# Performance work log

Measured on AMD Instinct MI355X. Metric: run time of the kernel, lower is better.

The kernel has to match this reference:

```python
import jax, jax.numpy as jnp
import numpy as np

B, S = 256, 512          # batch, seqlen
M = 128                  # memory_size
DK = 128                 # memory_key_state_dim == q_embed_dim == final_fc_dim
DV = 256                 # memory_value_state_dim == qa_embed_dim
NQ = 10000               # n_question
FC = 128                 # final_fc_dim


def _kaiming(key, shape):
    fan_in = shape[-1]
    return jax.random.normal(key, shape, dtype=jnp.float32) * np.float32(np.sqrt(2.0 / fan_in))


def setup_inputs() -> dict:
    key = jax.random.key(0)
    ks = jax.random.split(key, 12)
    q_data = jax.random.randint(ks[0], (B, S), 0, NQ + 1)
    qa_data = jax.random.randint(ks[1], (B, S), 0, 2 * NQ + 1)
    # embedding tables (padding_idx=0 -> zero row)
    q_embed_table = _kaiming(ks[2], (NQ + 1, DK)).at[0].set(0.0)
    qa_embed_table = _kaiming(ks[3], (2 * NQ + 1, DV)).at[0].set(0.0)
    memory_key = _kaiming(ks[4], (M, DK))
    init_memory_value = _kaiming(ks[5], (M, DV))
    W_erase = _kaiming(ks[6], (DV, DV)); b_erase = jnp.zeros((DV,), jnp.float32)
    W_add = _kaiming(ks[7], (DV, DV)); b_add = jnp.zeros((DV,), jnp.float32)
    W_read = _kaiming(ks[8], (FC, DV + FC)); b_read = jnp.zeros((FC,), jnp.float32)
    W_pred = _kaiming(ks[9], (1, FC)); b_pred = jnp.zeros((1,), jnp.float32)
    return {
        "q_data": q_data, "qa_data": qa_data,
        "q_embed_table": q_embed_table, "qa_embed_table": qa_embed_table,
        "memory_key": memory_key, "init_memory_value": init_memory_value,
        "W_erase": W_erase, "b_erase": b_erase,
        "W_add": W_add, "b_add": b_add,
        "W_read": W_read, "b_read": b_read,
        "W_pred": W_pred, "b_pred": b_pred,
    }


def reference(q_data, qa_data, q_embed_table, qa_embed_table, memory_key,
              init_memory_value, W_erase, b_erase, W_add, b_add,
              W_read, b_read, W_pred, b_pred):
    batch = q_data.shape[0]
    qe = q_embed_table[q_data]      # [B,S,DK]
    qae = qa_embed_table[qa_data]   # [B,S,DV]

    def step(mem, inp):
        q_t, qa_t = inp  # [B,DK], [B,DV]
        # key addressing: tiny matmul + softmax
        w = jax.nn.softmax(q_t @ memory_key.T, axis=1)            # [B,M]
        # weighted read from value memory
        read = jnp.einsum('bm,bmd->bd', w, mem)                   # [B,DV]
        # gated erase/add write
        e = jax.nn.sigmoid(qa_t @ W_erase.T + b_erase)            # [B,DV]
        a = jnp.tanh(qa_t @ W_add.T + b_add)                      # [B,DV]
        mem = mem * (1.0 - w[:, :, None] * e[:, None, :]) + w[:, :, None] * a[:, None, :]
        return mem, read

    mem0 = jnp.broadcast_to(init_memory_value, (batch,) + init_memory_value.shape)
    _, reads = jax.lax.scan(step, mem0, (qe.transpose(1, 0, 2), qae.transpose(1, 0, 2)))
    reads = reads.transpose(1, 0, 2)                              # [B,S,DV]

    predict_input = jnp.concatenate([reads, qe], axis=-1)         # [B,S,DV+FC]
    h = jnp.tanh(predict_input @ W_read.T + b_read)               # [B,S,FC]
    logits = h @ W_pred.T + b_pred                                # [B,S,1]
    return logits[..., 0]
```

## Files before the change

### kernel.cpp

```cpp
#include <hip/hip_runtime.h>
#include <hip/hip_bf16.h>


#define BB    256
#define SS    512
#define MM    128
#define DKk   128
#define DVv   256

typedef float  f32x2  __attribute__((ext_vector_type(2)));
typedef float  f32x4  __attribute__((ext_vector_type(4)));
typedef short  bf16x8 __attribute__((ext_vector_type(8)));

static __device__ __forceinline__ unsigned short f2bf(float f) {
    unsigned u = __float_as_uint(f);
    unsigned r = (u + 0x7FFFu + ((u >> 16) & 1u)) >> 16;
    return (unsigned short)r;
}
static __device__ __forceinline__ float fast_tanh(float x) {
    float ex = __expf(2.f * x);
    return 1.f - 2.f / (ex + 1.f);
}
static __device__ __forceinline__ float fast_sigmoid(float x) {
    return 1.f / (1.f + __expf(-x));
}

__global__ __launch_bounds__(256) void kt_transpose(const float* __restrict__ mk,
                                                    float* __restrict__ mkt) {
    int idx = blockIdx.x * 256 + threadIdx.x;
    int m = idx >> 7, k = idx & 127;
    mkt[(size_t)k * MM + m] = mk[(size_t)m * DKk + k];
}

__global__ __launch_bounds__(256) void kcvt(const float* __restrict__ qa_tab,
                                            const float* __restrict__ q_tab,
                                            const float* __restrict__ W_er,
                                            const float* __restrict__ W_ad,
                                            const float* __restrict__ W_rd,
                                            unsigned short* __restrict__ qa16,
                                            unsigned short* __restrict__ q16,
                                            unsigned short* __restrict__ wea16,
                                            unsigned short* __restrict__ wrd16,
                                            int n_qa, int n_q) {
    for (int i = blockIdx.x * 256 + threadIdx.x; i < n_qa; i += gridDim.x * 256)
        qa16[i] = f2bf(qa_tab[i]);
    for (int i = blockIdx.x * 256 + threadIdx.x; i < n_q; i += gridDim.x * 256)
        q16[i] = f2bf(q_tab[i]);
    for (int i = blockIdx.x * 256 + threadIdx.x; i < 65536; i += gridDim.x * 256) {
        wea16[i] = f2bf(W_er[i]);
        wea16[65536 + i] = f2bf(W_ad[i]);
    }
    for (int i = blockIdx.x * 256 + threadIdx.x; i < 49152; i += gridDim.x * 256)
        wrd16[i] = f2bf(W_rd[i]);
}

__global__ __launch_bounds__(256) void k1_scores(const int* __restrict__ q_data,
                                                 const float* __restrict__ q_tab,
                                                 const float* __restrict__ mkt,
                                                 float* __restrict__ w_buf,
                                                 int tcs, int tcm, int coff) {
    __shared__ float A[64][132];
    __shared__ int qidx[64];
    int t = threadIdx.x;
    int row0 = blockIdx.x * 64;
    if (t < 64) {
        int rl = row0 + t;
        qidx[t] = q_data[(rl >> tcs) * SS + coff + (rl & tcm)];
    }
    __syncthreads();
    #pragma unroll
    for (int i = 0; i < 8; ++i) {
        int f = t + 256 * i;
        int r = f >> 5, c4 = f & 31;
        float4 v = *reinterpret_cast<const float4*>(q_tab + (size_t)qidx[r] * DKk + c4 * 4);
        *reinterpret_cast<float4*>(&A[r][c4 * 4]) = v;
    }
    __syncthreads();
    int rg = t >> 4, cg = t & 15;
    float acc[4][8];
    #pragma unroll
    for (int i = 0; i < 4; ++i)
        #pragma unroll
        for (int j = 0; j < 8; ++j) acc[i][j] = 0.f;

    for (int k = 0; k < 128; k += 4) {
        float a_[4][4];
        #pragma unroll
        for (int i = 0; i < 4; ++i) {
            float4 v = *reinterpret_cast<const float4*>(&A[rg * 4 + i][k]);
            a_[i][0] = v.x; a_[i][1] = v.y; a_[i][2] = v.z; a_[i][3] = v.w;
        }
        #pragma unroll
        for (int kk = 0; kk < 4; ++kk) {
            const float* bp = mkt + (size_t)(k + kk) * MM + cg * 8;
            float4 b0 = *reinterpret_cast<const float4*>(bp);
            float4 b1 = *reinterpret_cast<const float4*>(bp + 4);
            #pragma unroll
            for (int i = 0; i < 4; ++i) {
                float av = a_[i][kk];
                acc[i][0] = fmaf(av, b0.x, acc[i][0]);
                acc[i][1] = fmaf(av, b0.y, acc[i][1]);
                acc[i][2] = fmaf(av, b0.z, acc[i][2]);
                acc[i][3] = fmaf(av, b0.w, acc[i][3]);
                acc[i][4] = fmaf(av, b1.x, acc[i][4]);
                acc[i][5] = fmaf(av, b1.y, acc[i][5]);
                acc[i][6] = fmaf(av, b1.z, acc[i][6]);
                acc[i][7] = fmaf(av, b1.w, acc[i][7]);
            }
        }
    }
    #pragma unroll
    for (int i = 0; i < 4; ++i) {
        float mx = acc[i][0];
        #pragma unroll
        for (int j = 1; j < 8; ++j) mx = fmaxf(mx, acc[i][j]);
        for (int off = 1; off < 16; off <<= 1) mx = fmaxf(mx, __shfl_xor(mx, off, 64));
        float s = 0.f;
        #pragma unroll
        for (int j = 0; j < 8; ++j) { float p = __expf(acc[i][j] - mx); acc[i][j] = p; s += p; }
        for (int off = 1; off < 16; off <<= 1) s += __shfl_xor(s, off, 64);
        float inv = 1.f / s;
        #pragma unroll
        for (int j = 0; j < 8; ++j) acc[i][j] *= inv;
        size_t ro = (size_t)(row0 + rg * 4 + i) * MM + cg * 8;
        *reinterpret_cast<float4*>(w_buf + ro)     = make_float4(acc[i][0], acc[i][1], acc[i][2], acc[i][3]);
        *reinterpret_cast<float4*>(w_buf + ro + 4) = make_float4(acc[i][4], acc[i][5], acc[i][6], acc[i][7]);
    }
}

__global__ __launch_bounds__(256) void k2_ea_mfma(const int* __restrict__ qa_data,
                                                  const unsigned short* __restrict__ qa16,
                                                  const unsigned short* __restrict__ wea16,
                                                  const float* __restrict__ b_er,
                                                  const float* __restrict__ b_ad,
                                                  float* __restrict__ ea_buf,
                                                  int tcs, int tcm, int coff) {
    __shared__ __align__(16) unsigned short A_lds[128 * 64];
    __shared__ int qidx[128];
    int t = threadIdx.x;
    int rb = blockIdx.x >> 2, cb = blockIdx.x & 3;
    int row0 = rb * 128;
    if (t < 128) {
        int rl = row0 + t;
        qidx[t] = qa_data[(rl >> tcs) * SS + coff + (rl & tcm)];
    }
    int l = t & 63;
    int wid = t >> 6, wr = wid >> 1, wc = wid & 1;
    f32x4 acc[4][4];
    #pragma unroll
    for (int i = 0; i < 4; ++i)
        #pragma unroll
        for (int j = 0; j < 4; ++j)
            acc[i][j] = (f32x4){0.f, 0.f, 0.f, 0.f};

    for (int ks = 0; ks < 256; ks += 64) {
        __syncthreads();
        #pragma unroll
        for (int p = 0; p < 4; ++p) {
            int U = p * 256 + t;
            int r = U >> 3, kb = U & 7;
            int kb_log = kb ^ (r & 7);
            int4 v = *reinterpret_cast<const int4*>(qa16 + (size_t)qidx[r] * 256 + ks + kb_log * 8);
            *reinterpret_cast<int4*>(&A_lds[U * 8]) = v;
        }
        __syncthreads();
        #pragma unroll
        for (int ksub = 0; ksub < 2; ++ksub) {
            bf16x8 af[4];
            #pragma unroll
            for (int mi = 0; mi < 4; ++mi) {
                int r = wr * 64 + mi * 16 + (l & 15);
                int kb_log = ksub * 4 + (l >> 4);
                int pu = r * 8 + (kb_log ^ (r & 7));
                af[mi] = *reinterpret_cast<const bf16x8*>(&A_lds[pu * 8]);
            }
            #pragma unroll
            for (int nj = 0; nj < 4; ++nj) {
                int col = cb * 128 + wc * 64 + nj * 16 + (l & 15);
                bf16x8 bf = *reinterpret_cast<const bf16x8*>(
                    wea16 + (size_t)col * 256 + ks + ksub * 32 + (l >> 4) * 8);
                #pragma unroll
                for (int mi = 0; mi < 4; ++mi)
                    acc[mi][nj] = __builtin_amdgcn_mfma_f32_16x16x32_bf16(af[mi], bf, acc[mi][nj], 0, 0, 0);
            }
        }
    }
    #pragma unroll
    for (int nj = 0; nj < 4; ++nj) {
        int col = cb * 128 + wc * 64 + nj * 16 + (l & 15);
        bool is_e = (cb < 2);
        float bias = is_e ? b_er[col] : b_ad[col - 256];
        #pragma unroll
        for (int mi = 0; mi < 4; ++mi) {
            #pragma unroll
            for (int reg = 0; reg < 4; ++reg) {
                int rl = row0 + wr * 64 + mi * 16 + (l >> 4) * 4 + reg;
                float x = acc[mi][nj][reg] + bias;
                float y = is_e ? fast_sigmoid(x) : fast_tanh(x);
                ea_buf[(size_t)rl * 512 + col] = y;
            }
        }
    }
}

__global__ __launch_bounds__(1024, 1) void k3_seq(const float* __restrict__ w_buf,
                                                  const float* __restrict__ ea_buf,
                                                  const float* __restrict__ init_mem,
                                                  float* __restrict__ state,
                                                  unsigned short* __restrict__ reads16,
                                                  int TC, int first, int last) {
    __shared__ float wlds[2][8][128];
    __shared__ float rdlds[8][4][256];
    int b = blockIdx.x;
    int tid = threadIdx.x;
    int wv = tid >> 6, lane = tid & 63;
    int mq = wv >> 2, dq = wv & 3;
    int d = dq * 64 + lane;
    int m0 = mq * 32;
    f32x2 mem[16];
    if (first) {
        #pragma unroll
        for (int i = 0; i < 16; ++i) {
            mem[i].x = init_mem[(size_t)(m0 + 2 * i) * DVv + d];
            mem[i].y = init_mem[(size_t)(m0 + 2 * i + 1) * DVv + d];
        }
    } else {
        #pragma unroll
        for (int i = 0; i < 16; ++i)
            mem[i] = *reinterpret_cast<const f32x2*>(&state[((size_t)b * DVv + d) * MM + m0 + 2 * i]);
    }
    size_t rb = (size_t)b * TC;
    int gg = tid >> 7, mm = tid & 127;
    wlds[0][gg][mm] = w_buf[(rb + gg) * MM + mm];
    __syncthreads();
    for (int t0 = 0; t0 < TC; t0 += 8) {
        int cur = (t0 >> 3) & 1, nxt = cur ^ 1;
        bool havenext = (t0 + 8) < TC;
        float wn = 0.f;
        if (havenext) wn = w_buf[(rb + t0 + 8 + gg) * MM + mm];
        float e8[8], a8[8];
        #pragma unroll
        for (int g = 0; g < 8; ++g) {
            size_t rr = (rb + t0 + g) * 512;
            e8[g] = ea_buf[rr + d];
            a8[g] = ea_buf[rr + 256 + d];
        }
        #pragma unroll
        for (int g = 0; g < 8; ++g) {
            const f32x4* wp4 = reinterpret_cast<const f32x4*>(&wlds[cur][g][m0]);
            f32x2 rd; rd.x = 0.f; rd.y = 0.f;
            f32x2 ne2; ne2.x = -e8[g]; ne2.y = -e8[g];
            f32x2 a2;  a2.x = a8[g];  a2.y = a8[g];
            #pragma unroll
            for (int j = 0; j < 8; ++j) {
                f32x4 w4 = wp4[j];
                f32x2 wlo; wlo.x = w4.x; wlo.y = w4.y;
                f32x2 whi; whi.x = w4.z; whi.y = w4.w;
                f32x2 tt;
                asm("v_pk_fma_f32 %0, %1, %2, %0" : "+v"(rd)          : "v"(wlo), "v"(mem[2*j]));
                asm("v_pk_fma_f32 %0, %1, %2, %3" : "=v"(tt)          : "v"(ne2), "v"(mem[2*j]), "v"(a2));
                asm("v_pk_fma_f32 %0, %1, %2, %0" : "+v"(mem[2*j])    : "v"(wlo), "v"(tt));
                asm("v_pk_fma_f32 %0, %1, %2, %0" : "+v"(rd)          : "v"(whi), "v"(mem[2*j+1]));
                asm("v_pk_fma_f32 %0, %1, %2, %3" : "=v"(tt)          : "v"(ne2), "v"(mem[2*j+1]), "v"(a2));
                asm("v_pk_fma_f32 %0, %1, %2, %0" : "+v"(mem[2*j+1])  : "v"(whi), "v"(tt));
            }
            rdlds[g][mq][d] = rd.x + rd.y;
        }
        __syncthreads();
        if (havenext) wlds[nxt][gg][mm] = wn;
        #pragma unroll
        for (int r = 0; r < 2; ++r) {
            int idx = tid + r * 1024;
            int g = idx >> 8, dd = idx & 255;
            float s = rdlds[g][0][dd] + rdlds[g][1][dd] + rdlds[g][2][dd] + rdlds[g][3][dd];
            reads16[(rb + t0 + g) * DVv + dd] = f2bf(s);
        }
        __syncthreads();
    }
    if (!last) {
        #pragma unroll
        for (int i = 0; i < 16; ++i)
            *reinterpret_cast<f32x2*>(&state[((size_t)b * DVv + d) * MM + m0 + 2 * i]) = mem[i];
    }
}

__global__ __launch_bounds__(256) void k4_mfma(const int* __restrict__ q_data,
                                               const unsigned short* __restrict__ q16,
                                               const unsigned short* __restrict__ reads16,
                                               const unsigned short* __restrict__ wrd16,
                                               const float* __restrict__ b_rd,
                                               const float* __restrict__ W_pr,
                                               const float* __restrict__ b_pr,
                                               float* __restrict__ out,
                                               int tcs, int tcm, int coff) {
    __shared__ __align__(16) unsigned short A_lds[128 * 64];
    __shared__ int qidx[128];
    __shared__ float plds[2][128];
    int t = threadIdx.x;
    int row0 = blockIdx.x * 128;
    if (t < 128) {
        int rl = row0 + t;
        qidx[t] = q_data[(rl >> tcs) * SS + coff + (rl & tcm)];
    }
    int l = t & 63;
    int wid = t >> 6, wr = wid >> 1, wc = wid & 1;
    f32x4 acc[4][4];
    #pragma unroll
    for (int i = 0; i < 4; ++i)
        #pragma unroll
        for (int j = 0; j < 4; ++j)
            acc[i][j] = (f32x4){0.f, 0.f, 0.f, 0.f};

    for (int ks = 0; ks < 384; ks += 64) {
        __syncthreads();
        #pragma unroll
        for (int p = 0; p < 4; ++p) {
            int U = p * 256 + t;
            int r = U >> 3, kb = U & 7;
            int kb_log = kb ^ (r & 7);
            int kg = ks + kb_log * 8;
            const unsigned short* src = (kg < 256)
                ? (reads16 + (size_t)(row0 + r) * DVv + kg)
                : (q16 + (size_t)qidx[r] * DKk + (kg - 256));
            int4 v = *reinterpret_cast<const int4*>(src);
            *reinterpret_cast<int4*>(&A_lds[U * 8]) = v;
        }
        __syncthreads();
        #pragma unroll
        for (int ksub = 0; ksub < 2; ++ksub) {
            bf16x8 af[4];
            #pragma unroll
            for (int mi = 0; mi < 4; ++mi) {
                int r = wr * 64 + mi * 16 + (l & 15);
                int kb_log = ksub * 4 + (l >> 4);
                int pu = r * 8 + (kb_log ^ (r & 7));
                af[mi] = *reinterpret_cast<const bf16x8*>(&A_lds[pu * 8]);
            }
            #pragma unroll
            for (int nj = 0; nj < 4; ++nj) {
                int col = wc * 64 + nj * 16 + (l & 15);
                bf16x8 bf = *reinterpret_cast<const bf16x8*>(
                    wrd16 + (size_t)col * 384 + ks + ksub * 32 + (l >> 4) * 8);
                #pragma unroll
                for (int mi = 0; mi < 4; ++mi)
                    acc[mi][nj] = __builtin_amdgcn_mfma_f32_16x16x32_bf16(af[mi], bf, acc[mi][nj], 0, 0, 0);
            }
        }
    }
    float part[16];
    #pragma unroll
    for (int k = 0; k < 16; ++k) part[k] = 0.f;
    #pragma unroll
    for (int nj = 0; nj < 4; ++nj) {
        int col = wc * 64 + nj * 16 + (l & 15);
        float bias = b_rd[col];
        float wpr = W_pr[col];
        #pragma unroll
        for (int mi = 0; mi < 4; ++mi) {
            #pragma unroll
            for (int reg = 0; reg < 4; ++reg) {
                float h = fast_tanh(acc[mi][nj][reg] + bias);
                part[mi * 4 + reg] = fmaf(h, wpr, part[mi * 4 + reg]);
            }
        }
    }
    #pragma unroll
    for (int k = 0; k < 16; ++k) {
        #pragma unroll
        for (int off = 1; off < 16; off <<= 1)
            part[k] += __shfl_xor(part[k], off, 64);
    }
    if ((l & 15) == 0) {
        #pragma unroll
        for (int mi = 0; mi < 4; ++mi)
            #pragma unroll
            for (int reg = 0; reg < 4; ++reg) {
                int row = wr * 64 + mi * 16 + (l >> 4) * 4 + reg;
                plds[wc][row] = part[mi * 4 + reg];
            }
    }
    __syncthreads();
    if (t < 128) {
        float s = plds[0][t] + plds[1][t] + b_pr[0];
        int rl = row0 + t;
        out[(rl >> tcs) * SS + coff + (rl & tcm)] = s;
    }
}

extern "C" void kernel_launch(void* const* d_in, const int* in_sizes, int n_in,
                              void* d_out, int out_size, void* d_ws, size_t ws_size,
                              hipStream_t stream) {
    const int*   q_data   = (const int*)d_in[0];
    const int*   qa_data  = (const int*)d_in[1];
    const float* q_tab    = (const float*)d_in[2];
    const float* qa_tab   = (const float*)d_in[3];
    const float* mk       = (const float*)d_in[4];
    const float* init_mem = (const float*)d_in[5];
    const float* W_er     = (const float*)d_in[6];
    const float* b_er     = (const float*)d_in[7];
    const float* W_ad     = (const float*)d_in[8];
    const float* b_ad     = (const float*)d_in[9];
    const float* W_rd     = (const float*)d_in[10];
    const float* b_rd     = (const float*)d_in[11];
    const float* W_pr     = (const float*)d_in[12];
    const float* b_pr     = (const float*)d_in[13];
    float* out = (float*)d_out;

    const size_t state_f = (size_t)BB * MM * DVv;
    const size_t qa16_n  = (size_t)in_sizes[3];
    const size_t q16_n   = (size_t)in_sizes[2];
    const size_t wea16_n = 131072;
    const size_t wrd16_n = 49152;
    const size_t bf16_f  = (qa16_n + q16_n + wea16_n + wrd16_n) / 2 + 16;

    size_t avail_f = ws_size / 4;
    int TC = 8;
    {
        const int cand[] = {512, 256, 128, 64, 32, 16, 8};
        for (int i = 0; i < 7; ++i) {
            size_t need = 16384 + state_f + bf16_f + (size_t)BB * cand[i] * (MM + 512 + 128);
            if (need <= avail_f) { TC = cand[i]; break; }
        }
    }
    int NC = SS / TC;
    int tcs = __builtin_ctz(TC);
    int tcm = TC - 1;

    float* ws      = (float*)d_ws;
    float* mkt     = ws;
    float* state   = mkt + 16384;
    float* w_buf   = state + state_f;
    float* ea_buf  = w_buf + (size_t)BB * TC * MM;
    unsigned short* reads16 = (unsigned short*)(ea_buf + (size_t)BB * TC * 512);
    unsigned short* qa16  = reads16 + (size_t)BB * TC * DVv;
    unsigned short* q16   = qa16 + qa16_n;
    unsigned short* wea16 = q16 + q16_n;
    unsigned short* wrd16 = wea16 + wea16_n;

    kt_transpose<<<64, 256, 0, stream>>>(mk, mkt);
    kcvt<<<1024, 256, 0, stream>>>(qa_tab, q_tab, W_er, W_ad, W_rd, qa16, q16, wea16, wrd16,
                                   (int)qa16_n, (int)q16_n);
    for (int c = 0; c < NC; ++c) {
        int coff = c * TC;
        int rows = BB * TC;
        k1_scores<<<rows / 64, 256, 0, stream>>>(q_data, q_tab, mkt, w_buf, tcs, tcm, coff);
        k2_ea_mfma<<<(rows / 128) * 4, 256, 0, stream>>>(qa_data, qa16, wea16, b_er, b_ad,
                                                         ea_buf, tcs, tcm, coff);
        k3_seq<<<BB, 1024, 0, stream>>>(w_buf, ea_buf, init_mem, state, reads16,
                                        TC, c == 0, c == NC - 1);
        k4_mfma<<<rows / 128, 256, 0, stream>>>(q_data, q16, reads16, wrd16, b_rd, W_pr, b_pr,
                                                out, tcs, tcm, coff);
    }
}
```

Measured before the change: 625.9 us.

## Use MFMA for key scores, bf16 erase/add buffer, readlane weights in scan

```diff
diff --git a/kernel.cpp b/kernel.cpp
--- a/kernel.cpp
+++ b/kernel.cpp
@@ -17,19 +17,15 @@
     unsigned r = (u + 0x7FFFu + ((u >> 16) & 1u)) >> 16;
     return (unsigned short)r;
 }
+static __device__ __forceinline__ float bf2f(unsigned short u) {
+    return __uint_as_float(((unsigned)u) << 16);
+}
 static __device__ __forceinline__ float fast_tanh(float x) {
     float ex = __expf(2.f * x);
     return 1.f - 2.f / (ex + 1.f);
 }
 static __device__ __forceinline__ float fast_sigmoid(float x) {
     return 1.f / (1.f + __expf(-x));
-}
-
-__global__ __launch_bounds__(256) void kt_transpose(const float* __restrict__ mk,
-                                                    float* __restrict__ mkt) {
-    int idx = blockIdx.x * 256 + threadIdx.x;
-    int m = idx >> 7, k = idx & 127;
-    mkt[(size_t)k * MM + m] = mk[(size_t)m * DKk + k];
 }
 
 __global__ __launch_bounds__(256) void kcvt(const float* __restrict__ qa_tab,
@@ -37,10 +33,12 @@
                                             const float* __restrict__ W_er,
                                             const float* __restrict__ W_ad,
                                             const float* __restrict__ W_rd,
+                                            const float* __restrict__ mk,
                                             unsigned short* __restrict__ qa16,
                                             unsigned short* __restrict__ q16,
                                             unsigned short* __restrict__ wea16,
                                             unsigned short* __restrict__ wrd16,
+                                            unsigned short* __restrict__ mk16,
                                             int n_qa, int n_q) {
     for (int i = blockIdx.x * 256 + threadIdx.x; i < n_qa; i += gridDim.x * 256)
         qa16[i] = f2bf(qa_tab[i]);
@@ -52,79 +50,84 @@
     }
     for (int i = blockIdx.x * 256 + threadIdx.x; i < 49152; i += gridDim.x * 256)
         wrd16[i] = f2bf(W_rd[i]);
-}
-
-__global__ __launch_bounds__(256) void k1_scores(const int* __restrict__ q_data,
-                                                 const float* __restrict__ q_tab,
-                                                 const float* __restrict__ mkt,
-                                                 float* __restrict__ w_buf,
-                                                 int tcs, int tcm, int coff) {
-    __shared__ float A[64][132];
-    __shared__ int qidx[64];
+    for (int i = blockIdx.x * 256 + threadIdx.x; i < 16384; i += gridDim.x * 256)
+        mk16[i] = f2bf(mk[i]);
+}
+
+__global__ __launch_bounds__(256) void k1_mfma(const int* __restrict__ q_data,
+                                               const unsigned short* __restrict__ q16,
+                                               const unsigned short* __restrict__ mk16,
+                                               float* __restrict__ w_buf,
+                                               int tcs, int tcm, int coff) {
+    __shared__ __align__(16) unsigned short A_lds[128 * 64];
+    __shared__ int qidx[128];
     int t = threadIdx.x;
-    int row0 = blockIdx.x * 64;
-    if (t < 64) {
+    int row0 = blockIdx.x * 128;
+    if (t < 128) {
         int rl = row0 + t;
         qidx[t] = q_data[(rl >> tcs) * SS + coff + (rl & tcm)];
     }
-    __syncthreads();
-    #pragma unroll
-    for (int i = 0; i < 8; ++i) {
-        int f = t + 256 * i;
-        int r = f >> 5, c4 = f & 31;
-        float4 v = *reinterpret_cast<const float4*>(q_tab + (size_t)qidx[r] * DKk + c4 * 4);
-        *reinterpret_cast<float4*>(&A[r][c4 * 4]) = v;
-    }
-    __syncthreads();
-    int rg = t >> 4, cg = t & 15;
-    float acc[4][8];
-    #pragma unroll
-    for (int i = 0; i < 4; ++i)
-        #pragma unroll
-        for (int j = 0; j < 8; ++j) acc[i][j] = 0.f;
-
-    for (int k = 0; k < 128; k += 4) {
-        float a_[4][4];
-        #pragma unroll
-        for (int i = 0; i < 4; ++i) {
-            float4 v = *reinterpret_cast<const float4*>(&A[rg * 4 + i][k]);
-            a_[i][0] = v.x; a_[i][1] = v.y; a_[i][2] = v.z; a_[i][3] = v.w;
-        }
-        #pragma unroll
-        for (int kk = 0; kk < 4; ++kk) {
-            const float* bp = mkt + (size_t)(k + kk) * MM + cg * 8;
-            float4 b0 = *reinterpret_cast<const float4*>(bp);
-            float4 b1 = *reinterpret_cast<const float4*>(bp + 4);
-            #pragma unroll
-            for (int i = 0; i < 4; ++i) {
-                float av = a_[i][kk];
-                acc[i][0] = fmaf(av, b0.x, acc[i][0]);
-                acc[i][1] = fmaf(av, b0.y, acc[i][1]);
-                acc[i][2] = fmaf(av, b0.z, acc[i][2]);
-                acc[i][3] = fmaf(av, b0.w, acc[i][3]);
-                acc[i][4] = fmaf(av, b1.x, acc[i][4]);
-                acc[i][5] = fmaf(av, b1.y, acc[i][5]);
-                acc[i][6] = fmaf(av, b1.z, acc[i][6]);
-                acc[i][7] = fmaf(av, b1.w, acc[i][7]);
-            }
-        }
-    }
-    #pragma unroll
-    for (int i = 0; i < 4; ++i) {
-        float mx = acc[i][0];
-        #pragma unroll
-        for (int j = 1; j < 8; ++j) mx = fmaxf(mx, acc[i][j]);
-        for (int off = 1; off < 16; off <<= 1) mx = fmaxf(mx, __shfl_xor(mx, off, 64));
-        float s = 0.f;
-        #pragma unroll
-        for (int j = 0; j < 8; ++j) { float p = __expf(acc[i][j] - mx); acc[i][j] = p; s += p; }
-        for (int off = 1; off < 16; off <<= 1) s += __shfl_xor(s, off, 64);
-        float inv = 1.f / s;
-        #pragma unroll
-        for (int j = 0; j < 8; ++j) acc[i][j] *= inv;
-        size_t ro = (size_t)(row0 + rg * 4 + i) * MM + cg * 8;
-        *reinterpret_cast<float4*>(w_buf + ro)     = make_float4(acc[i][0], acc[i][1], acc[i][2], acc[i][3]);
-        *reinterpret_cast<float4*>(w_buf + ro + 4) = make_float4(acc[i][4], acc[i][5], acc[i][6], acc[i][7]);
+    int l = t & 63;
+    int wid = t >> 6;
+    f32x4 acc[2][8];
+    #pragma unroll
+    for (int i = 0; i < 2; ++i)
+        #pragma unroll
+        for (int j = 0; j < 8; ++j)
+            acc[i][j] = (f32x4){0.f, 0.f, 0.f, 0.f};
+
+    for (int ks = 0; ks < 128; ks += 64) {
+        __syncthreads();
+        #pragma unroll
+        for (int p = 0; p < 4; ++p) {
+            int U = p * 256 + t;
+            int r = U >> 3, kb = U & 7;
+            int kb_log = kb ^ (r & 7);
+            int4 v = *reinterpret_cast<const int4*>(q16 + (size_t)qidx[r] * DKk + ks + kb_log * 8);
+            *reinterpret_cast<int4*>(&A_lds[U * 8]) = v;
+        }
+        __syncthreads();
+        #pragma unroll
+        for (int ksub = 0; ksub < 2; ++ksub) {
+            bf16x8 af[2];
+            #pragma unroll
+            for (int mi = 0; mi < 2; ++mi) {
+                int r = wid * 32 + mi * 16 + (l & 15);
+                int kb_log = ksub * 4 + (l >> 4);
+                int pu = r * 8 + (kb_log ^ (r & 7));
+                af[mi] = *reinterpret_cast<const bf16x8*>(&A_lds[pu * 8]);
+            }
+            #pragma unroll
+            for (int nj = 0; nj < 8; ++nj) {
+                int col = nj * 16 + (l & 15);
+                bf16x8 bf = *reinterpret_cast<const bf16x8*>(
+                    mk16 + (size_t)col * DKk + ks + ksub * 32 + (l >> 4) * 8);
+                #pragma unroll
+                for (int mi = 0; mi < 2; ++mi)
+                    acc[mi][nj] = __builtin_amdgcn_mfma_f32_16x16x32_bf16(af[mi], bf, acc[mi][nj], 0, 0, 0);
+            }
+        }
+    }
+    #pragma unroll
+    for (int mi = 0; mi < 2; ++mi) {
+        #pragma unroll
+        for (int reg = 0; reg < 4; ++reg) {
+            float mx = acc[mi][0][reg];
+            #pragma unroll
+            for (int nj = 1; nj < 8; ++nj) mx = fmaxf(mx, acc[mi][nj][reg]);
+            #pragma unroll
+            for (int off = 1; off < 16; off <<= 1) mx = fmaxf(mx, __shfl_xor(mx, off, 64));
+            float p[8], s = 0.f;
+            #pragma unroll
+            for (int nj = 0; nj < 8; ++nj) { p[nj] = __expf(acc[mi][nj][reg] - mx); s += p[nj]; }
+            #pragma unroll
+            for (int off = 1; off < 16; off <<= 1) s += __shfl_xor(s, off, 64);
+            float inv = 1.f / s;
+            int row = row0 + wid * 32 + mi * 16 + (l >> 4) * 4 + reg;
+            #pragma unroll
+            for (int nj = 0; nj < 8; ++nj)
+                w_buf[(size_t)row * MM + nj * 16 + (l & 15)] = p[nj] * inv;
+        }
     }
 }
 
@@ -133,7 +136,7 @@
                                                   const unsigned short* __restrict__ wea16,
                                                   const float* __restrict__ b_er,
                                                   const float* __restrict__ b_ad,
-                                                  float* __restrict__ ea_buf,
+                                                  unsigned short* __restrict__ ea16,
                                                   int tcs, int tcm, int coff) {
     __shared__ __align__(16) unsigned short A_lds[128 * 64];
     __shared__ int qidx[128];
@@ -197,19 +200,18 @@
                 int rl = row0 + wr * 64 + mi * 16 + (l >> 4) * 4 + reg;
                 float x = acc[mi][nj][reg] + bias;
                 float y = is_e ? fast_sigmoid(x) : fast_tanh(x);
-                ea_buf[(size_t)rl * 512 + col] = y;
+                ea16[(size_t)rl * 512 + col] = f2bf(y);
             }
         }
     }
 }
 
 __global__ __launch_bounds__(1024, 1) void k3_seq(const float* __restrict__ w_buf,
-                                                  const float* __restrict__ ea_buf,
+                                                  const unsigned short* __restrict__ ea16,
                                                   const float* __restrict__ init_mem,
                                                   float* __restrict__ state,
                                                   unsigned short* __restrict__ reads16,
                                                   int TC, int first, int last) {
-    __shared__ float wlds[2][8][128];
     __shared__ float rdlds[8][4][256];
     int b = blockIdx.x;
     int tid = threadIdx.x;
@@ -230,44 +232,36 @@
             mem[i] = *reinterpret_cast<const f32x2*>(&state[((size_t)b * DVv + d) * MM + m0 + 2 * i]);
     }
     size_t rb = (size_t)b * TC;
-    int gg = tid >> 7, mm = tid & 127;
-    wlds[0][gg][mm] = w_buf[(rb + gg) * MM + mm];
-    __syncthreads();
     for (int t0 = 0; t0 < TC; t0 += 8) {
-        int cur = (t0 >> 3) & 1, nxt = cur ^ 1;
-        bool havenext = (t0 + 8) < TC;
-        float wn = 0.f;
-        if (havenext) wn = w_buf[(rb + t0 + 8 + gg) * MM + mm];
+        f32x4 w4 = *reinterpret_cast<const f32x4*>(
+            w_buf + (rb + t0 + (lane >> 3)) * MM + m0 + (lane & 7) * 4);
         float e8[8], a8[8];
         #pragma unroll
         for (int g = 0; g < 8; ++g) {
-            size_t rr = (rb + t0 + g) * 512;
-            e8[g] = ea_buf[rr + d];
-            a8[g] = ea_buf[rr + 256 + d];
+            const unsigned short* ep = ea16 + (rb + t0 + g) * 512;
+            e8[g] = bf2f(ep[d]);
+            a8[g] = bf2f(ep[256 + d]);
         }
         #pragma unroll
         for (int g = 0; g < 8; ++g) {
-            const f32x4* wp4 = reinterpret_cast<const f32x4*>(&wlds[cur][g][m0]);
             f32x2 rd; rd.x = 0.f; rd.y = 0.f;
             f32x2 ne2; ne2.x = -e8[g]; ne2.y = -e8[g];
             f32x2 a2;  a2.x = a8[g];  a2.y = a8[g];
             #pragma unroll
-            for (int j = 0; j < 8; ++j) {
-                f32x4 w4 = wp4[j];
-                f32x2 wlo; wlo.x = w4.x; wlo.y = w4.y;
-                f32x2 whi; whi.x = w4.z; whi.y = w4.w;
+            for (int i = 0; i < 16; ++i) {
+                int src = 8 * g + (i >> 1);
+                int c = (i & 1) * 2;
+                f32x2 ws;
+                ws.x = __uint_as_float((unsigned)__builtin_amdgcn_readlane(__float_as_uint(w4[c]), src));
+                ws.y = __uint_as_float((unsigned)__builtin_amdgcn_readlane(__float_as_uint(w4[c + 1]), src));
                 f32x2 tt;
-                asm("v_pk_fma_f32 %0, %1, %2, %0" : "+v"(rd)          : "v"(wlo), "v"(mem[2*j]));
-                asm("v_pk_fma_f32 %0, %1, %2, %3" : "=v"(tt)          : "v"(ne2), "v"(mem[2*j]), "v"(a2));
-                asm("v_pk_fma_f32 %0, %1, %2, %0" : "+v"(mem[2*j])    : "v"(wlo), "v"(tt));
-                asm("v_pk_fma_f32 %0, %1, %2, %0" : "+v"(rd)          : "v"(whi), "v"(mem[2*j+1]));
-                asm("v_pk_fma_f32 %0, %1, %2, %3" : "=v"(tt)          : "v"(ne2), "v"(mem[2*j+1]), "v"(a2));
-                asm("v_pk_fma_f32 %0, %1, %2, %0" : "+v"(mem[2*j+1])  : "v"(whi), "v"(tt));
+                asm("v_pk_fma_f32 %0, %1, %2, %0" : "+v"(rd)     : "s"(ws), "v"(mem[i]));
+                asm("v_pk_fma_f32 %0, %1, %2, %3" : "=v"(tt)     : "v"(ne2), "v"(mem[i]), "v"(a2));
+                asm("v_pk_fma_f32 %0, %1, %2, %0" : "+v"(mem[i]) : "s"(ws), "v"(tt));
             }
             rdlds[g][mq][d] = rd.x + rd.y;
         }
         __syncthreads();
-        if (havenext) wlds[nxt][gg][mm] = wn;
         #pragma unroll
         for (int r = 0; r < 2; ++r) {
             int idx = tid + r * 1024;
@@ -411,14 +405,15 @@
     const size_t q16_n   = (size_t)in_sizes[2];
     const size_t wea16_n = 131072;
     const size_t wrd16_n = 49152;
-    const size_t bf16_f  = (qa16_n + q16_n + wea16_n + wrd16_n) / 2 + 16;
+    const size_t mk16_n  = 16384;
+    const size_t bf16_f  = (qa16_n + q16_n + wea16_n + wrd16_n + mk16_n) / 2 + 32;
 
     size_t avail_f = ws_size / 4;
     int TC = 8;
     {
         const int cand[] = {512, 256, 128, 64, 32, 16, 8};
         for (int i = 0; i < 7; ++i) {
-            size_t need = 16384 + state_f + bf16_f + (size_t)BB * cand[i] * (MM + 512 + 128);
+            size_t need = state_f + bf16_f + (size_t)BB * cand[i] * (MM + 256 + 128);
             if (need <= avail_f) { TC = cand[i]; break; }
         }
     }
@@ -427,26 +422,26 @@
     int tcm = TC - 1;
 
     float* ws      = (float*)d_ws;
-    float* mkt     = ws;
-    float* state   = mkt + 16384;
+    float* state   = ws;
     float* w_buf   = state + state_f;
-    float* ea_buf  = w_buf + (size_t)BB * TC * MM;
-    unsigned short* reads16 = (unsigned short*)(ea_buf + (size_t)BB * TC * 512);
+    unsigned short* ea16    = (unsigned short*)(w_buf + (size_t)BB * TC * MM);
+    unsigned short* reads16 = ea16 + (size_t)BB * TC * 512;
     unsigned short* qa16  = reads16 + (size_t)BB * TC * DVv;
     unsigned short* q16   = qa16 + qa16_n;
     unsigned short* wea16 = q16 + q16_n;
     unsigned short* wrd16 = wea16 + wea16_n;
-
-    kt_transpose<<<64, 256, 0, stream>>>(mk, mkt);
-    kcvt<<<1024, 256, 0, stream>>>(qa_tab, q_tab, W_er, W_ad, W_rd, qa16, q16, wea16, wrd16,
+    unsigned short* mk16  = wrd16 + wrd16_n;
+
+    kcvt<<<1024, 256, 0, stream>>>(qa_tab, q_tab, W_er, W_ad, W_rd, mk,
+                                   qa16, q16, wea16, wrd16, mk16,
                                    (int)qa16_n, (int)q16_n);
     for (int c = 0; c < NC; ++c) {
         int coff = c * TC;
         int rows = BB * TC;
-        k1_scores<<<rows / 64, 256, 0, stream>>>(q_data, q_tab, mkt, w_buf, tcs, tcm, coff);
+        k1_mfma<<<rows / 128, 256, 0, stream>>>(q_data, q16, mk16, w_buf, tcs, tcm, coff);
         k2_ea_mfma<<<(rows / 128) * 4, 256, 0, stream>>>(qa_data, qa16, wea16, b_er, b_ad,
-                                                         ea_buf, tcs, tcm, coff);
-        k3_seq<<<BB, 1024, 0, stream>>>(w_buf, ea_buf, init_mem, state, reads16,
+                                                         ea16, tcs, tcm, coff);
+        k3_seq<<<BB, 1024, 0, stream>>>(w_buf, ea16, init_mem, state, reads16,
                                         TC, c == 0, c == NC - 1);
         k4_mfma<<<rows / 128, 256, 0, stream>>>(q_data, q16, reads16, wrd16, b_rd, W_pr, b_pr,
                                                 out, tcs, tcm, coff);
```

New measurement: 609.9 us. 1.03x faster.
